# Kernel optimization log

Measured on AMD Instinct MI355X. Metric: run time of the kernel, lower is better.

## Reference

```python
import jax, jax.numpy as jnp
import numpy as np

# NTU RGB+D 25-joint skeleton edges (1-based)
NTU_EDGES = [(1,2),(2,21),(3,21),(4,3),(5,21),(6,5),(7,6),(8,7),(9,21),(10,9),
             (11,10),(12,11),(13,1),(14,13),(15,14),(16,15),(17,1),(18,17),
             (19,18),(20,19),(22,23),(23,8),(24,25),(25,12)]
NUM_SCALES = 13
NUM_POINT = 25


def build_A_powers(num_scales=NUM_SCALES, v=NUM_POINT):
    # MS-G3D disentangled multi-scale aggregation: exact-k-hop adjacencies, each
    # with self loops, symmetrically normalized, stacked along dim 0 -> (K*V, V).
    A = np.zeros((v, v))
    for i, j in NTU_EDGES:
        A[i - 1, j - 1] = 1.0
        A[j - 1, i - 1] = 1.0
    I = np.eye(v)
    mats = []
    for k in range(num_scales):
        if k == 0:
            Ak = I.copy()
        else:
            Ak = np.minimum(np.linalg.matrix_power(A + I, k), 1) \
               - np.minimum(np.linalg.matrix_power(A + I, k - 1), 1)
            Ak = Ak + I  # with_self=True
        d = Ak.sum(-1)
        dinv = np.where(d > 0, d ** -0.5, 0.0)
        mats.append((dinv[:, None] * Ak) * dinv[None, :])
    return np.concatenate(mats, 0).astype(np.float32)


def batchnorm(x, g, b, axes, ch_axis, eps=1e-5):
    # torch BatchNorm in training mode: biased batch stats + affine
    mean = jnp.mean(x, axes, keepdims=True)
    var = jnp.mean((x - mean) ** 2, axes, keepdims=True)
    shape = [1] * x.ndim
    shape[ch_axis] = -1
    return (x - mean) * jax.lax.rsqrt(var + eps) * g.reshape(shape) + b.reshape(shape)


def ms_gcn(x, A_powers, A_res, W, b, g, beta, num_scales):
    # x: (N, C, T, V); A: (K*V, V)
    A = A_powers + A_res
    support = jnp.einsum('vu,nctu->nctv', A, x)            # (N, C, T, K*V)
    N, C, T, KV = support.shape
    V = KV // num_scales
    support = support.reshape(N, C, T, num_scales, V).transpose(0, 3, 1, 2, 4)
    support = support.reshape(N, num_scales * C, T, V)     # (N, K*C, T, V)
    out = jnp.einsum('oc,nctv->notv', W, support) + b[None, :, None, None]  # 1x1 conv
    out = batchnorm(out, g, beta, (0, 2, 3), 1)
    return jax.nn.relu(out)


def lstm(x, Wih, Whh, bih, bhh):
    # single-layer batch_first LSTM, zero initial state; torch gate order i,f,g,o
    B = x.shape[0]
    H = Whh.shape[1]
    xp = jnp.einsum('bsd,hd->bsh', x, Wih) + bih + bhh     # precompute input proj

    def step(carry, xt):
        h, c = carry
        gates = xt + h @ Whh.T
        i, f, g, o = jnp.split(gates, 4, axis=-1)
        c = jax.nn.sigmoid(f) * c + jax.nn.sigmoid(i) * jnp.tanh(g)
        h = jax.nn.sigmoid(o) * jnp.tanh(c)
        return (h, c), h

    init = (jnp.zeros((B, H), x.dtype), jnp.zeros((B, H), x.dtype))
    _, ys = jax.lax.scan(step, init, jnp.swapaxes(xp, 0, 1))
    return jnp.swapaxes(ys, 0, 1)                          # (B, S, H)


def logsig_rnn(x, n_segments, Wih, Whh, bih, bhh):
    # x: (B, T, d). Depth-2 log-signature per time segment + segment start point,
    # concatenated and fed to an LSTM (Logsig-RNN layer).
    B, T, d = x.shape
    t_vec = np.array([int(round(float(v))) for v in np.linspace(1, T, n_segments + 1)])
    starts = t_vec[:-1] - 1
    ends = t_vec[1:] - 1
    L = int((ends - starts).max()) + 1
    # pad segments to fixed length by repeating the last point (zero increments)
    idx = np.minimum(starts[:, None] + np.arange(L)[None, :], ends[:, None])  # (S, L)
    pts = x[:, idx, :]                                     # (B, S, L, d)
    rel = pts - pts[:, :, :1, :]
    inc = rel[:, :, -1, :]                                 # level-1: total increment
    dx = pts[:, :, 1:, :] - pts[:, :, :-1, :]
    Mm = jnp.einsum('bsli,bslj->bsij', rel[:, :, :-1, :], dx)
    iu, ju = np.triu_indices(d, k=1)
    levy = 0.5 * (Mm[:, :, iu, ju] - Mm[:, :, ju, iu])     # level-2 (Lyndon basis)
    feats = jnp.concatenate([x[:, starts, :], inc, levy], axis=-1)
    return lstm(feats, Wih, Whh, bih, bhh)


def setup_inputs() -> dict:
    key = jax.random.key(0)
    ks = iter(jax.random.split(key, 16))
    N, C, T, V, M = 2, 3, 100, 25, 2
    c1, c2, num_class, K = 96, 192, 60, NUM_SCALES

    def randn(shape, scale):
        return jax.random.normal(next(ks), shape, jnp.float32) * scale

    ls1 = c1 + c1 * (c1 - 1) // 2     # 4656
    ls2 = c2 + c2 * (c2 - 1) // 2     # 18528
    in1 = c1 + ls1                    # 4752
    in2 = c2 + ls2                    # 18720
    Ap = jnp.asarray(build_A_powers())
    return {
        'x': jax.random.normal(next(ks), (N, C, T, V, M), jnp.float32),
        'length': jax.random.randint(next(ks), (N,), 0, T),
        'data_bn_g': jnp.ones((M * V * C,)), 'data_bn_b': jnp.zeros((M * V * C,)),
        'A_powers1': Ap,
        'A_res1': jax.random.uniform(next(ks), Ap.shape, jnp.float32, -1e-6, 1e-6),
        'W1': randn((c1, K * C), (K * C) ** -0.5), 'b1': jnp.zeros((c1,)),
        'bn1_g': jnp.ones((c1,)), 'bn1_b': jnp.zeros((c1,)),
        'Wih1': randn((4 * c1, in1), in1 ** -0.5), 'Whh1': randn((4 * c1, c1), c1 ** -0.5),
        'bih1': jnp.zeros((4 * c1,)), 'bhh1': jnp.zeros((4 * c1,)),
        'bnseg1_g': jnp.ones((50,)), 'bnseg1_b': jnp.zeros((50,)),
        'A_powers2': Ap,
        'A_res2': jax.random.uniform(next(ks), Ap.shape, jnp.float32, -1e-6, 1e-6),
        'W2': randn((c2, K * c1), (K * c1) ** -0.5), 'b2': jnp.zeros((c2,)),
        'bn2_g': jnp.ones((c2,)), 'bn2_b': jnp.zeros((c2,)),
        'Wih2': randn((4 * c2, in2), in2 ** -0.5), 'Whh2': randn((4 * c2, c2), c2 ** -0.5),
        'bih2': jnp.zeros((4 * c2,)), 'bhh2': jnp.zeros((4 * c2,)),
        'bnseg2_g': jnp.ones((30,)), 'bnseg2_b': jnp.zeros((30,)),
        'fcW': randn((num_class, c2), c2 ** -0.5), 'fcb': jnp.zeros((num_class,)),
    }


def reference(x, length, data_bn_g, data_bn_b, A_powers1, A_res1, W1, b1, bn1_g, bn1_b,
              Wih1, Whh1, bih1, bhh1, bnseg1_g, bnseg1_b, A_powers2, A_res2, W2, b2,
              bn2_g, bn2_b, Wih2, Whh2, bih2, bhh2, bnseg2_g, bnseg2_b, fcW, fcb):
    # `length` is accepted but unused, as in the original forward.
    N, C, T, V, M = x.shape
    K = A_powers1.shape[0] // V
    c1, c2 = W1.shape[0], W2.shape[0]
    S1, S2 = 50, 30

    h = x.transpose(0, 4, 3, 1, 2).reshape(N, M * V * C, T)
    h = batchnorm(h, data_bn_g, data_bn_b, (0, 2), 1)
    h = h.reshape(N * M, V, C, T).transpose(0, 2, 3, 1)            # (NM, C, T, V)

    h = jax.nn.relu(ms_gcn(h, A_powers1, A_res1, W1, b1, bn1_g, bn1_b, K))
    h = h.transpose(0, 3, 2, 1).reshape(N * M * V, T, c1)
    h = logsig_rnn(h, S1, Wih1, Whh1, bih1, bhh1)                  # (NMV, S1, c1)
    h = batchnorm(h, bnseg1_g, bnseg1_b, (0, 2), 1)
    h = h.reshape(N * M, V, S1, c1).transpose(0, 3, 2, 1)          # (NM, c1, S1, V)

    h = jax.nn.relu(ms_gcn(h, A_powers2, A_res2, W2, b2, bn2_g, bn2_b, K))
    h = h.transpose(0, 3, 2, 1).reshape(N * M * V, S1, c2)
    h = logsig_rnn(h, S2, Wih2, Whh2, bih2, bhh2)                  # (NMV, S2, c2)
    h = batchnorm(h, bnseg2_g, bnseg2_b, (0, 2), 1)
    h = h.reshape(N * M, V, S2, c2).transpose(0, 3, 2, 1)          # (NM, c2, S2, V)

    pooled = h.reshape(N, M, c2, -1).mean(axis=3).mean(axis=1)     # (N, c2)
    return pooled @ fcW.T + fcb
```

## Files before the change

### kernel.cpp

```cpp
#include <hip/hip_runtime.h>
#include <cmath>
#include <cstdint>
#include <cstddef>

typedef unsigned short bf16_t;
typedef __attribute__((ext_vector_type(8))) short short8;
typedef __attribute__((ext_vector_type(4))) float floatx4;
typedef __attribute__((ext_vector_type(2))) _Float16 half2_t;
typedef __attribute__((ext_vector_type(8))) _Float16 half8_t;

__device__ __forceinline__ float bf2f(bf16_t b){
  unsigned int u = ((unsigned int)b) << 16;
  return __uint_as_float(u);
}
__device__ __forceinline__ bf16_t f2bf(float f){
  unsigned int u = __float_as_uint(f);
  unsigned int r = (u + 0x7fffu + ((u >> 16) & 1u)) >> 16;
  return (bf16_t)r;
}
__device__ __forceinline__ unsigned int f2bf2(float a, float b){
  return (unsigned int)f2bf(a) | ((unsigned int)f2bf(b) << 16);
}
__device__ __forceinline__ float sigf(float x){ return 1.0f / (1.0f + expf(-x)); }

__device__ __forceinline__ float dot2(half2_t a, half2_t b, float c){
#if __has_builtin(__builtin_amdgcn_fdot2)
  return __builtin_amdgcn_fdot2(a, b, c, false);
#else
  return c + (float)a.x * (float)b.x + (float)a.y * (float)b.y;
#endif
}

__device__ __forceinline__ void gload_lds16(const bf16_t* g, bf16_t* lds){
  __builtin_amdgcn_global_load_lds(
      (const __attribute__((address_space(1))) unsigned int*)g,
      (__attribute__((address_space(3))) unsigned int*)lds, 16, 0, 0);
}

__device__ __forceinline__ void barrier_raw(){
  asm volatile("s_barrier" ::: "memory");
}

__device__ __forceinline__ int xcd_chunk_swizzle(int orig, int nwg){
  int q = nwg >> 3, r = nwg & 7;
  int xcd = orig & 7, idx = orig >> 3;
  return (xcd < r ? xcd * (q + 1) : r * (q + 1) + (xcd - r) * q) + idx;
}

__global__ void prep_misc(const float* __restrict__ a1, const float* __restrict__ r1, float* __restrict__ o1,
                          const float* __restrict__ a2, const float* __restrict__ r2, float* __restrict__ o2,
                          const float* __restrict__ bi1, const float* __restrict__ bh1, float* __restrict__ ob1,
                          const float* __restrict__ bi2, const float* __restrict__ bh2, float* __restrict__ ob2,
                          const float* __restrict__ Whh1, half2_t* __restrict__ Wp1,
                          const float* __restrict__ Whh2, half2_t* __restrict__ Wp2,
                          unsigned short* __restrict__ lut1, unsigned short* __restrict__ lut2,
                          float* __restrict__ stats, bf16_t* __restrict__ A2mat){
  int i = blockIdx.x * blockDim.x + threadIdx.x;
  if (i < 8125){ o1[i] = a1[i] + r1[i]; o2[i] = a2[i] + r2[i]; }
  if (i < 384) ob1[i] = bi1[i] + bh1[i];
  if (i < 768) ob2[i] = bi2[i] + bh2[i];
  if (i < 736) stats[i] = 0.f;
  if (i < 18432){
    int t = i % 384, j2 = i / 384;
    half2_t w; w.x = (_Float16)Whh1[(size_t)t * 96 + 2 * j2];
    w.y = (_Float16)Whh1[(size_t)t * 96 + 2 * j2 + 1];
    Wp1[i] = w;
  }
  if (i < 73728){
    int t = i % 768, j2 = i / 768;
    half2_t w; w.x = (_Float16)Whh2[(size_t)t * 192 + 2 * j2];
    w.y = (_Float16)Whh2[(size_t)t * 192 + 2 * j2 + 1];
    Wp2[i] = w;
  }
  if (i < 4560){
    int d = 96, p = i;
    int r = (int)(((2.0 * d - 1.0) - sqrt((2.0 * d - 1.0) * (2.0 * d - 1.0) - 8.0 * (double)p)) * 0.5);
    if (r < 0) r = 0;
    while (r + 1 <= d - 2 && (r + 1) * (d - 1) - ((r + 1) * r) / 2 <= p) ++r;
    while (r > 0 && r * (d - 1) - (r * (r - 1)) / 2 > p) --r;
    int jj = p - (r * (d - 1) - (r * (r - 1)) / 2);
    lut1[p] = (unsigned short)((r << 8) | (r + 1 + jj));
  }
  if (i < 18336){
    int d = 192, p = i;
    int r = (int)(((2.0 * d - 1.0) - sqrt((2.0 * d - 1.0) * (2.0 * d - 1.0) - 8.0 * (double)p)) * 0.5);
    if (r < 0) r = 0;
    while (r + 1 <= d - 2 && (r + 1) * (d - 1) - ((r + 1) * r) / 2 <= p) ++r;
    while (r > 0 && r * (d - 1) - (r * (r - 1)) / 2 > p) --r;
    int jj = p - (r * (d - 1) - (r * (r - 1)) / 2);
    lut2[p] = (unsigned short)((r << 8) | (r + 1 + jj));
  }
  if (i < 160000){
    int row = i >> 5, col = 1248 + (i & 31);
    A2mat[(size_t)row * 1280 + col] = 0;
  }
}

__device__ __forceinline__ void f2bf_seg(const float* in, bf16_t* out, int Kin, int Kout, int li){
  int ko8 = Kout >> 3;
  int r = li / ko8, k8 = (li % ko8) << 3;
  uint4 u;
  if (k8 + 8 <= Kin){
    const float4* p = reinterpret_cast<const float4*>(in + (size_t)r * Kin + k8);
    float4 x0 = p[0], x1 = p[1];
    u.x = f2bf2(x0.x, x0.y); u.y = f2bf2(x0.z, x0.w);
    u.z = f2bf2(x1.x, x1.y); u.w = f2bf2(x1.z, x1.w);
  } else {
    u.x = u.y = u.z = u.w = 0u;
  }
  *reinterpret_cast<uint4*>(out + (size_t)r * Kout + k8) = u;
}

__global__ void f2bf_pad8_3(const float* __restrict__ in1, bf16_t* __restrict__ out1, int Kin1, int Kout1, int c1,
                            const float* __restrict__ in2, bf16_t* __restrict__ out2, int Kin2, int Kout2, int c2,
                            const float* __restrict__ in3, bf16_t* __restrict__ out3, int Kin3, int Kout3, int c3){
  int idx = blockIdx.x * blockDim.x + threadIdx.x;
  if (idx < c1){ f2bf_seg(in1, out1, Kin1, Kout1, idx); return; }
  idx -= c1;
  if (idx < c2){ f2bf_seg(in2, out2, Kin2, Kout2, idx); return; }
  idx -= c2;
  if (idx < c3) f2bf_seg(in3, out3, Kin3, Kout3, idx);
}

__global__ void data_bn_kernel(const float* __restrict__ x, const float* __restrict__ g,
                               const float* __restrict__ bb, float* __restrict__ h1,
                               int N, int C, int T, int V, int M){
  int ch = blockIdx.x;
  int m = ch / (V * C);
  int v = (ch / C) % V;
  int c = ch % C;
  int tid = threadIdx.x;
  int cnt = N * T;
  float s = 0.f, s2 = 0.f;
  for (int i = tid; i < cnt; i += 64){
    int n = i / T, t = i % T;
    float val = x[(((size_t)(n * C + c) * T + t) * V + v) * M + m];
    s += val; s2 += val * val;
  }
  for (int off = 32; off; off >>= 1){ s += __shfl_down(s, off); s2 += __shfl_down(s2, off); }
  s = __shfl(s, 0); s2 = __shfl(s2, 0);
  float mean = s / cnt;
  float rstd = rsqrtf(s2 / cnt - mean * mean + 1e-5f);
  float gg = g[ch], bo = bb[ch];
  for (int i = tid; i < cnt; i += 64){
    int n = i / T, t = i % T;
    float val = x[(((size_t)(n * C + c) * T + t) * V + v) * M + m];
    float y = (val - mean) * rstd * gg + bo;
    h1[((size_t)((n * M + m) * C + c) * T + t) * V + v] = y;
  }
}

__global__ __launch_bounds__(256)
void gcn1_fused(const float* __restrict__ A, const float* __restrict__ h1,
                const float* __restrict__ W1, const float* __restrict__ b1,
                float* __restrict__ y1, float* __restrict__ ssum, float* __restrict__ ssq, int T){
  __shared__ float h[3][25];
  __shared__ float sup[3][325];
  __shared__ float lsum[96], lsq[96];
  int blk = blockIdx.x;
  int nm = blk / T, t = blk % T;
  int tid = threadIdx.x;
  if (tid < 75){
    int c = tid / 25, v = tid % 25;
    h[c][v] = h1[((size_t)(nm * 3 + c) * T + t) * 25 + v];
  }
  if (tid < 96){ lsum[tid] = 0.f; lsq[tid] = 0.f; }
  __syncthreads();
  for (int w = tid; w < 975; w += 256){
    int c = w / 325, ww = w % 325;
    const float* ar = A + ww * 25;
    float acc = 0.f;
    #pragma unroll
    for (int u = 0; u < 25; ++u) acc += ar[u] * h[c][u];
    sup[c][ww] = acc;
  }
  __syncthreads();
  for (int o2 = tid; o2 < 2400; o2 += 256){
    int v = o2 / 96, o = o2 % 96;
    float acc = b1[o];
    #pragma unroll
    for (int k = 0; k < 13; ++k)
      #pragma unroll
      for (int c = 0; c < 3; ++c)
        acc += W1[o * 39 + k * 3 + c] * sup[c][k * 25 + v];
    y1[((size_t)blk * 25 + v) * 96 + o] = acc;
    atomicAdd(&lsum[o], acc);
    atomicAdd(&lsq[o], acc * acc);
  }
  __syncthreads();
  if (tid < 96){ atomicAdd(&ssum[tid], lsum[tid]); atomicAdd(&ssq[tid], lsq[tid]); }
}

struct SegTable { int st[50]; int en[50]; };

__global__ void feats_bn_kernel(const float* __restrict__ ymat, const float* __restrict__ sum,
                                const float* __restrict__ sumsq, const float* __restrict__ g,
                                const float* __restrict__ bb, bf16_t* __restrict__ feats,
                                SegTable segs, const unsigned int* __restrict__ lut32,
                                int T, int d, int S, int L, int pairs, int rowlenP, int R){
  __shared__ float pts[4][192];
  int bs = blockIdx.x;
  int b = bs / S, s = bs % S;
  int nm = b / 25, v = b % 25;
  int st = segs.st[s], en = segs.en[s];
  int nt = blockDim.x, tid = threadIdx.x;
  for (int l = 0; l < L; ++l){
    int t = st + l; if (t > en) t = en;
    const float* yrow = ymat + ((size_t)(nm * T + t) * 25 + v) * d;
    for (int i = tid; i < d; i += nt){
      float mean = sum[i] / R;
      float rstd = rsqrtf(sumsq[i] / R - mean * mean + 1e-5f);
      pts[l][i] = fmaxf((yrow[i] - mean) * rstd * g[i] + bb[i], 0.f);
    }
  }
  __syncthreads();
  unsigned int* frow32 = reinterpret_cast<unsigned int*>(feats + (size_t)bs * rowlenP);
  int d2 = d >> 1;
  for (int i2 = tid; i2 < d2; i2 += nt){
    int i = 2 * i2;
    frow32[i2]      = f2bf2(pts[0][i], pts[0][i + 1]);
    frow32[d2 + i2] = f2bf2(pts[L - 1][i] - pts[0][i], pts[L - 1][i + 1] - pts[0][i + 1]);
  }
  int rowlen2 = (2 * d + pairs) >> 1, rowlenP2 = rowlenP >> 1;
  for (int i = tid + rowlen2; i < rowlenP2; i += nt) frow32[i] = 0;
  int Lm2 = L - 2;
  unsigned int* lrow32 = frow32 + d;
  int pairs2 = pairs >> 1;
  for (int p2 = tid; p2 < pairs2; p2 += nt){
    unsigned int ee = lut32[p2];
    int i0 = (ee >> 8) & 255, j0 = ee & 255;
    int i1 = ee >> 24, j1 = (ee >> 16) & 255;
    float acc0 = 0.f, acc1 = 0.f;
    for (int l = 1; l <= Lm2; ++l){
      float ri = pts[l][i0] - pts[0][i0], rj = pts[l][j0] - pts[0][j0];
      float di = pts[l + 1][i0] - pts[l][i0], dj = pts[l + 1][j0] - pts[l][j0];
      acc0 += ri * dj - rj * di;
      float ri1 = pts[l][i1] - pts[0][i1], rj1 = pts[l][j1] - pts[0][j1];
      float di1 = pts[l + 1][i1] - pts[l][i1], dj1 = pts[l + 1][j1] - pts[l][j1];
      acc1 += ri1 * dj1 - rj1 * di1;
    }
    lrow32[p2] = f2bf2(0.5f * acc0, 0.5f * acc1);
  }
}

__global__ __launch_bounds__(256)
void gemm_mfma_nt_split(const bf16_t* __restrict__ A, const bf16_t* __restrict__ B,
                        float* __restrict__ P, int M, int N, int K,
                        int GX, int GY, int GZ){
  __shared__ bf16_t As[128 * 64];
  __shared__ bf16_t Bs[128 * 64];
  const int nwg = GX * GY * GZ;
  const int wg = xcd_chunk_swizzle(blockIdx.x, nwg);
  const int bxi = wg % GX, byi = (wg / GX) % GY, bzi = wg / (GX * GY);
  const int tid = threadIdx.x;
  const int lane = tid & 63, wv = tid >> 6;
  const int bm = bxi * 128, bn = byi * 128;
  const int wr = (wv >> 1) * 64, wc = (wv & 1) * 64;
  const int m_l = lane & 15, q = lane >> 4;

  const int ksteps = K >> 6;
  const int Z = GZ, z = bzi;
  const int per = (ksteps + Z - 1) / Z;
  const int ks0 = z * per;
  const int ks1 = (ks0 + per < ksteps) ? ks0 + per : ksteps;

  const int rlane = lane >> 3;
  const int slane = lane & 7;
  const int colc = (slane ^ rlane) * 8;
  const bf16_t* gA[4]; const bf16_t* gB[4];
  bf16_t* lA[4]; bf16_t* lB[4];
  #pragma unroll
  for (int it = 0; it < 4; ++it){
    int c = it * 4 + wv;
    int rowA = bm + c * 8 + rlane; if (rowA > M - 1) rowA = M - 1;
    int rowB = bn + c * 8 + rlane; if (rowB > N - 1) rowB = N - 1;
    gA[it] = A + (size_t)rowA * K + colc;
    gB[it] = B + (size_t)rowB * K + colc;
    lA[it] = &As[c * 512];
    lB[it] = &Bs[c * 512];
  }
  const int sxor = m_l & 7;

  floatx4 acc[4][4] = {};
  for (int ks = ks0; ks < ks1; ++ks){
    int k0 = ks << 6;
    __syncthreads();
    #pragma unroll
    for (int it = 0; it < 4; ++it){
      gload_lds16(gA[it] + k0, lA[it]);
      gload_lds16(gB[it] + k0, lB[it]);
    }
    __syncthreads();
    #pragma unroll
    for (int half = 0; half < 2; ++half){
      const int scol = ((half * 4 + q) ^ sxor) * 8;
      short8 af[4], bfr[4];
      #pragma unroll
      for (int i = 0; i < 4; ++i){
        af[i]  = *reinterpret_cast<const short8*>(&As[(wr + i * 16 + m_l) * 64 + scol]);
        bfr[i] = *reinterpret_cast<const short8*>(&Bs[(wc + i * 16 + m_l) * 64 + scol]);
      }
      #pragma unroll
      for (int mi = 0; mi < 4; ++mi)
        #pragma unroll
        for (int ni = 0; ni < 4; ++ni)
          acc[mi][ni] = __builtin_amdgcn_mfma_f32_16x16x32_bf16(af[mi], bfr[ni], acc[mi][ni], 0, 0, 0);
    }
  }

  float* Pz = P + (size_t)z * M * N;
  #pragma unroll
  for (int mi = 0; mi < 4; ++mi){
    int row0 = bm + wr + mi * 16 + q * 4;
    #pragma unroll
    for (int r = 0; r < 4; ++r){
      int row = row0 + r;
      if (row < M){
        #pragma unroll
        for (int ni = 0; ni < 4; ++ni){
          int col = bn + wc + ni * 16 + m_l;
          if (col < N) Pz[(size_t)row * N + col] = acc[mi][ni][r];
        }
      }
    }
  }
}

#define VMC4 asm volatile("s_waitcnt vmcnt(4)" ::: "memory")
#define VMC0 asm volatile("s_waitcnt vmcnt(0)" ::: "memory")
#define STG4(NB, KH, OFF) { gload_lds16(pA0 + (OFF) + (KH) * 32, dA0 + (NB) * 16384 + (KH) * 8192); \
                            gload_lds16(pA1 + (OFF) + (KH) * 32, dA1 + (NB) * 16384 + (KH) * 8192); \
                            gload_lds16(pB0 + (OFF) + (KH) * 32, dB0 + (NB) * 16384 + (KH) * 8192); \
                            gload_lds16(pB1 + (OFF) + (KH) * 32, dB1 + (NB) * 16384 + (KH) * 8192); }
#define HP(BUF, KH, STAGE_BLOCK, WAIT_BLOCK) { \
    const bf16_t* ab_ = As + (BUF) * 16384 + (KH) * 8192 + sA; \
    _Pragma("unroll") \
    for (int i_ = 0; i_ < 8; ++i_) af[i_] = *reinterpret_cast<const short8*>(ab_ + i_ * 512); \
    const bf16_t* bb_ = Bs + (BUF) * 16384 + (KH) * 8192 + sB; \
    _Pragma("unroll") \
    for (int i_ = 0; i_ < 4; ++i_) bfr[i_] = *reinterpret_cast<const short8*>(bb_ + i_ * 512); \
    STAGE_BLOCK; \
    WAIT_BLOCK; \
    barrier_raw(); \
    __builtin_amdgcn_s_setprio(1); \
    _Pragma("unroll") \
    for (int mi_ = 0; mi_ < 8; ++mi_) \
      _Pragma("unroll") \
      for (int ni_ = 0; ni_ < 4; ++ni_) \
        acc[mi_][ni_] = __builtin_amdgcn_mfma_f32_16x16x32_bf16(af[mi_], bfr[ni_], acc[mi_][ni_], 0, 0, 0); \
    __builtin_amdgcn_s_setprio(0); \
  }

__global__ __launch_bounds__(512, 2)
void gemm_mfma_nt_8ph(const bf16_t* __restrict__ A, const bf16_t* __restrict__ B,
                      float* __restrict__ P, int M, int N, int K,
                      int GX, int GY, int GZ){
  __shared__ bf16_t As[32768];
  __shared__ bf16_t Bs[32768];
  const int nwg = GX * GY * GZ;
  const int wg = xcd_chunk_swizzle(blockIdx.x, nwg);
  const int bxi = wg % GX, byi = (wg / GX) % GY, bzi = wg / (GX * GY);
  const int tid = threadIdx.x;
  const int lane = tid & 63, wv = tid >> 6;
  const int wm = wv >> 2, wn = wv & 3;
  const int m_l = lane & 15, q = lane >> 4;
  const int bm = bxi * 256, bn = byi * 256;

  const int ksteps = K >> 6;
  const int z = bzi, Z = GZ;
  const int per = (ksteps + Z - 1) / Z;
  const int ks0 = z * per;
  int ks1 = ks0 + per; if (ks1 > ksteps) ks1 = ksteps;
  if (ks0 >= ks1) return;

  const int rlane = lane >> 2, slane = lane & 3;
  const int cg = slane ^ ((rlane >> 1) & 3);
  int rr0 = wv * 16 + rlane, rr1 = (8 + wv) * 16 + rlane;
  int ra0 = bm + rr0; if (ra0 > M - 1) ra0 = M - 1;
  int ra1 = bm + rr1; if (ra1 > M - 1) ra1 = M - 1;
  int rb0 = bn + rr0; if (rb0 > N - 1) rb0 = N - 1;
  int rb1 = bn + rr1; if (rb1 > N - 1) rb1 = N - 1;
  const bf16_t* pA0 = A + (size_t)ra0 * K + cg * 8 + ks0 * 64;
  const bf16_t* pA1 = A + (size_t)ra1 * K + cg * 8 + ks0 * 64;
  const bf16_t* pB0 = B + (size_t)rb0 * K + cg * 8 + ks0 * 64;
  const bf16_t* pB1 = B + (size_t)rb1 * K + cg * 8 + ks0 * 64;
  bf16_t* dA0 = As + wv * 512;
  bf16_t* dA1 = As + (8 + wv) * 512;
  bf16_t* dB0 = Bs + wv * 512;
  bf16_t* dB1 = Bs + (8 + wv) * 512;

  const int sA = (wm * 128 + m_l) * 32 + ((q ^ ((m_l >> 1) & 3)) * 8);
  const int sB = (wn * 64 + m_l) * 32 + ((q ^ ((m_l >> 1) & 3)) * 8);

  short8 af[8], bfr[4];
  floatx4 acc[8][4] = {};

  STG4(0, 0, 0); STG4(0, 1, 0);
  VMC4;
  barrier_raw();

  int buf = 0;
  for (int t = ks0; t < ks1 - 1; ++t){
    const int nb = buf ^ 1;
    HP(buf, 0, STG4(nb, 0, 64), VMC4);
    HP(buf, 1, STG4(nb, 1, 64), VMC4);
    pA0 += 64; pA1 += 64; pB0 += 64; pB1 += 64;
    buf = nb;
  }
  HP(buf, 0, ((void)0), VMC0);
  HP(buf, 1, ((void)0), ((void)0));

  float* Pz = P + (size_t)z * M * N;
  #pragma unroll
  for (int mi = 0; mi < 8; ++mi){
    int row0 = bm + wm * 128 + mi * 16 + q * 4;
    #pragma unroll
    for (int r = 0; r < 4; ++r){
      int row = row0 + r;
      if (row < M){
        #pragma unroll
        for (int ni = 0; ni < 4; ++ni){
          int col = bn + wn * 64 + ni * 16 + m_l;
          if (col < N) Pz[(size_t)row * N + col] = acc[mi][ni][r];
        }
      }
    }
  }
}

__global__ __launch_bounds__(256)
void reduce_split_bias_stats(const float* __restrict__ P, const float* __restrict__ bias,
                             float* __restrict__ out, float* __restrict__ ssum, float* __restrict__ ssq,
                             int MN, int N, int Z){
  __shared__ float lsum[192], lsq[192];
  int tid = threadIdx.x;
  if (tid < 192){ lsum[tid] = 0.f; lsq[tid] = 0.f; }
  __syncthreads();
  int i4 = (blockIdx.x * blockDim.x + tid) * 4;
  if (i4 < MN){
    const float4 bv = *reinterpret_cast<const float4*>(bias + (i4 % N));
    float4 s = bv;
    for (int z = 0; z < Z; ++z){
      const float4 p = *reinterpret_cast<const float4*>(P + (size_t)z * MN + i4);
      s.x += p.x; s.y += p.y; s.z += p.z; s.w += p.w;
    }
    *reinterpret_cast<float4*>(out + i4) = s;
    int c0 = i4 % N;
    atomicAdd(&lsum[c0],     s.x); atomicAdd(&lsq[c0],     s.x * s.x);
    atomicAdd(&lsum[c0 + 1], s.y); atomicAdd(&lsq[c0 + 1], s.y * s.y);
    atomicAdd(&lsum[c0 + 2], s.z); atomicAdd(&lsq[c0 + 2], s.z * s.z);
    atomicAdd(&lsum[c0 + 3], s.w); atomicAdd(&lsq[c0 + 3], s.w * s.w);
  }
  __syncthreads();
  if (tid < 192){ atomicAdd(&ssum[tid], lsum[tid]); atomicAdd(&ssq[tid], lsq[tid]); }
}

template <int H2C, int BLK, int Z>
__global__ __launch_bounds__(BLK, 1)
void lstm_kernel(const float* __restrict__ P, const float* __restrict__ bias,
                 const half2_t* __restrict__ Wp, float* __restrict__ out,
                 int S, int MN){
  constexpr int H = 2 * H2C;
  constexpr int H4 = 4 * H;
  __shared__ _Float16 __attribute__((aligned(16))) hsh[H];
  __shared__ float gv[H4];
  __shared__ float av[H4];
  const int b = blockIdx.x, t = threadIdx.x;
  half2_t w[H2C];
  const half2_t* wp = Wp + t;
  #pragma unroll
  for (int j2 = 0; j2 < H2C; ++j2) w[j2] = wp[(size_t)j2 * H4];
  float cc = 0.f;
  if (t < H) hsh[t] = (_Float16)0.f;
  const float bval = bias[t];
  const size_t base = (size_t)b * S * H4 + t;
  float pv0[Z], pv1[Z];
  #pragma unroll
  for (int z = 0; z < Z; ++z) pv0[z] = P[(size_t)z * MN + base];
  #pragma unroll
  for (int z = 0; z < Z; ++z) pv1[z] = P[(size_t)z * MN + base + H4];
  __syncthreads();
  const half8_t* hp8 = reinterpret_cast<const half8_t*>(hsh);
  for (int s = 0; s < S; ++s){
    float pvn[Z];
    if (s + 2 < S){
      size_t o2 = base + (size_t)(s + 2) * H4;
      #pragma unroll
      for (int z = 0; z < Z; ++z) pvn[z] = P[(size_t)z * MN + o2];
    }
    float a0 = bval, a1 = 0.f, a2 = 0.f, a3 = 0.f;
    float a4 = 0.f, a5 = 0.f, a6 = 0.f, a7 = 0.f;
    #pragma unroll
    for (int z = 0; z < Z; ++z) a0 += pv0[z];
    #pragma unroll
    for (int j8 = 0; j8 < H2C / 8; ++j8){
      half8_t hv0 = hp8[2 * j8];
      half8_t hv1 = hp8[2 * j8 + 1];
      half2_t h0, h1, h2, h3, h4, h5, h6, h7;
      h0.x = hv0[0]; h0.y = hv0[1];
      h1.x = hv0[2]; h1.y = hv0[3];
      h2.x = hv0[4]; h2.y = hv0[5];
      h3.x = hv0[6]; h3.y = hv0[7];
      h4.x = hv1[0]; h4.y = hv1[1];
      h5.x = hv1[2]; h5.y = hv1[3];
      h6.x = hv1[4]; h6.y = hv1[5];
      h7.x = hv1[6]; h7.y = hv1[7];
      const int jb = 8 * j8;
      a0 = dot2(w[jb],     h0, a0);
      a1 = dot2(w[jb + 1], h1, a1);
      a2 = dot2(w[jb + 2], h2, a2);
      a3 = dot2(w[jb + 3], h3, a3);
      a4 = dot2(w[jb + 4], h4, a4);
      a5 = dot2(w[jb + 5], h5, a5);
      a6 = dot2(w[jb + 6], h6, a6);
      a7 = dot2(w[jb + 7], h7, a7);
    }
    gv[t] = ((a0 + a1) + (a2 + a3)) + ((a4 + a5) + (a6 + a7));
    __syncthreads();
    {
      float x = gv[t];
      av[t] = (t >= 2 * H && t < 3 * H) ? tanhf(x) : sigf(x);
    }
    __syncthreads();
    if (t < H){
      float ig = av[t];
      float fg = av[H + t];
      float gg = av[2 * H + t];
      float og = av[3 * H + t];
      cc = fg * cc + ig * gg;
      float hh = og * tanhf(cc);
      hsh[t] = (_Float16)hh;
      out[((size_t)b * S + s) * H + t] = hh;
    }
    __syncthreads();
    #pragma unroll
    for (int z = 0; z < Z; ++z){ pv0[z] = pv1[z]; pv1[z] = pvn[z]; }
  }
}

__global__ __launch_bounds__(256)
void seg_stats_kernel(const float* __restrict__ lout, float* __restrict__ ssum,
                      float* __restrict__ ssq, int S, int H, int B){
  int s = blockIdx.x;
  int tid = threadIdx.x;
  int cnt = B * H;
  float a = 0.f, b2 = 0.f;
  for (int i = tid; i < cnt; i += 256){
    int b = i / H, o = i % H;
    float v = lout[((size_t)b * S + s) * H + o];
    a += v; b2 += v * v;
  }
  for (int off = 32; off; off >>= 1){ a += __shfl_down(a, off); b2 += __shfl_down(b2, off); }
  __shared__ float sa[4], sb[4];
  int wid = tid >> 6, lane = tid & 63;
  if (lane == 0){ sa[wid] = a; sb[wid] = b2; }
  __syncthreads();
  if (tid == 0){
    ssum[s] = (sa[0] + sa[1]) + (sa[2] + sa[3]);
    ssq[s]  = (sb[0] + sb[1]) + (sb[2] + sb[3]);
  }
}

__global__ void support2_bn(const float* __restrict__ A, const float* __restrict__ lout,
                            const float* __restrict__ ssum, const float* __restrict__ ssq,
                            const float* __restrict__ g, const float* __restrict__ bb,
                            bf16_t* __restrict__ A2mat, int S, int cnt){
  int idx = blockIdx.x * blockDim.x + threadIdx.x;
  int total = 4 * S * 25 * 13 * 96;
  if (idx >= total) return;
  int c = idx % 96;
  int k = (idx / 96) % 13;
  int v = (idx / (96 * 13)) % 25;
  int rs = idx / (96 * 13 * 25);
  int s = rs % S, nm = rs / S;
  float mean = ssum[s] / cnt;
  float rstd = rsqrtf(ssq[s] / cnt - mean * mean + 1e-5f);
  float scale = rstd * g[s];
  float shift = bb[s] - mean * scale;
  const float* ar = A + (k * 25 + v) * 25;
  float acc = 0.f;
  #pragma unroll
  for (int u = 0; u < 25; ++u){
    float raw = lout[((size_t)(nm * 25 + u) * S + s) * 96 + c];
    acc += ar[u] * (raw * scale + shift);
  }
  A2mat[((size_t)rs * 25 + v) * 1280 + k * 96 + c] = f2bf(acc);
}

__global__ void pool_kernel(const float* __restrict__ lout2, const float* __restrict__ sum,
                            const float* __restrict__ sumsq, const float* __restrict__ g,
                            const float* __restrict__ bb, float* __restrict__ pooled,
                            int S, int H, int scnt){
  int n = blockIdx.x / H;
  int o = blockIdx.x % H;
  float acc = 0.f;
  int cnt = 2 * 25 * S;
  for (int i = threadIdx.x; i < cnt; i += 64){
    int m = i / (25 * S);
    int r = i % (25 * S);
    int v = r / S;
    int s = r % S;
    int b = (n * 2 + m) * 25 + v;
    float val = lout2[((size_t)b * S + s) * H + o];
    float mean = sum[s] / scnt;
    float rstd = rsqrtf(sumsq[s] / scnt - mean * mean + 1e-5f);
    val = (val - mean) * rstd * g[s] + bb[s];
    acc += val;
  }
  for (int off = 32; off; off >>= 1) acc += __shfl_down(acc, off);
  if (threadIdx.x == 0) pooled[n * H + o] = acc / cnt;
}

__global__ void fc_kernel(const float* __restrict__ pooled, const float* __restrict__ fcW,
                          const float* __restrict__ fcb, float* __restrict__ outp){
  int idx = blockIdx.x * blockDim.x + threadIdx.x;
  if (idx >= 120) return;
  int n = idx / 60, cls = idx % 60;
  float acc = fcb[cls];
  for (int o = 0; o < 192; ++o) acc += pooled[n * 192 + o] * fcW[cls * 192 + o];
  outp[idx] = acc;
}

static void make_segs(int T, int S, SegTable& tab, int& L){
  double step = (double)(T - 1) / (double)S;
  long long tv[51];
  for (int i = 0; i <= S; ++i){
    double v = 1.0 + step * (double)i;
    tv[i] = llrint(v);
  }
  L = 0;
  for (int s = 0; s < S; ++s){
    tab.st[s] = (int)tv[s] - 1;
    tab.en[s] = (int)tv[s + 1] - 1;
    int len = tab.en[s] - tab.st[s] + 1;
    if (len > L) L = len;
  }
  for (int s = S; s < 50; ++s){ tab.st[s] = 0; tab.en[s] = 0; }
  if (L > 4) L = 4;
}

extern "C" void kernel_launch(void* const* d_in, const int* in_sizes, int n_in,
                              void* d_out, int out_size, void* d_ws, size_t ws_size,
                              hipStream_t stream){
  const float* x         = (const float*)d_in[0];
  const float* data_bn_g = (const float*)d_in[2];
  const float* data_bn_b = (const float*)d_in[3];
  const float* A_powers1 = (const float*)d_in[4];
  const float* A_res1    = (const float*)d_in[5];
  const float* W1        = (const float*)d_in[6];
  const float* b1        = (const float*)d_in[7];
  const float* bn1_g     = (const float*)d_in[8];
  const float* bn1_b     = (const float*)d_in[9];
  const float* Wih1      = (const float*)d_in[10];
  const float* Whh1      = (const float*)d_in[11];
  const float* bih1      = (const float*)d_in[12];
  const float* bhh1      = (const float*)d_in[13];
  const float* bnseg1_g  = (const float*)d_in[14];
  const float* bnseg1_b  = (const float*)d_in[15];
  const float* A_powers2 = (const float*)d_in[16];
  const float* A_res2    = (const float*)d_in[17];
  const float* W2        = (const float*)d_in[18];
  const float* b2        = (const float*)d_in[19];
  const float* bn2_g     = (const float*)d_in[20];
  const float* bn2_b     = (const float*)d_in[21];
  const float* Wih2      = (const float*)d_in[22];
  const float* Whh2      = (const float*)d_in[23];
  const float* bih2      = (const float*)d_in[24];
  const float* bhh2      = (const float*)d_in[25];
  const float* bnseg2_g  = (const float*)d_in[26];
  const float* bnseg2_b  = (const float*)d_in[27];
  const float* fcW       = (const float*)d_in[28];
  const float* fcb       = (const float*)d_in[29];
  float* out = (float*)d_out;

  const int N = 2, C = 3, T = 100, V = 25, M = 2, NM = 4;
  const int C1 = 96, C2 = 192;
  const int S1 = 50, S2 = 30;
  const int B = 100;
  const int IN1 = 4752, IN2 = 18720;
  const int IN1P = 4800, IN2P = 18752;
  const int P1 = 4560, P2 = 18336;
  const int KG2 = 1248, KG2P = 1280;
  const int Z1 = 6, Z2 = 7, ZG = 4;

  size_t off = 0;
  char* base = (char*)d_ws;
  auto alloc = [&](size_t nbytes) -> void* {
    off = (off + 255) & ~(size_t)255;
    void* p = base + off;
    off += nbytes;
    return p;
  };
  float* A1full = (float*)alloc(325 * 25 * 4);
  float* A2full = (float*)alloc(325 * 25 * 4);
  float* h1     = (float*)alloc((size_t)NM * C * T * V * 4);
  float* y1mat  = (float*)alloc((size_t)NM * T * V * C1 * 4);
  float* stats  = (float*)alloc(736 * 4);
  float* st1a = stats, *st1b = stats + 96;
  float* sg1a = stats + 192, *sg1b = stats + 242;
  float* st2a = stats + 292, *st2b = stats + 484;
  float* sg2a = stats + 676, *sg2b = stats + 706;
  float* l1out  = (float*)alloc((size_t)B * S1 * C1 * 4);
  bf16_t* A2mat = (bf16_t*)alloc((size_t)NM * S1 * V * KG2P * 2);
  float* y2mat  = (float*)alloc((size_t)NM * S1 * V * C2 * 4);
  float* l2out  = (float*)alloc((size_t)B * S2 * C2 * 4);
  float* pooled = (float*)alloc(2 * C2 * 4);
  float* bias1  = (float*)alloc(4 * C1 * 4);
  float* bias2  = (float*)alloc(4 * C2 * 4);
  half2_t* Wp1  = (half2_t*)alloc((size_t)(C1 / 2) * 4 * C1 * 4);
  half2_t* Wp2  = (half2_t*)alloc((size_t)(C2 / 2) * 4 * C2 * 4);
  bf16_t* Wih1b = (bf16_t*)alloc((size_t)4 * C1 * IN1P * 2);
  bf16_t* Wih2b = (bf16_t*)alloc((size_t)4 * C2 * IN2P * 2);
  bf16_t* W2b   = (bf16_t*)alloc((size_t)C2 * KG2P * 2);
  unsigned short* lut1 = (unsigned short*)alloc((size_t)P1 * 2);
  unsigned short* lut2 = (unsigned short*)alloc((size_t)P2 * 2);
  size_t pmax = (size_t)Z2 * 3000 * 768;
  {
    size_t p1s = (size_t)Z1 * 5000 * 384; if (p1s > pmax) pmax = p1s;
    size_t pgs = (size_t)ZG * 5000 * 192; if (pgs > pmax) pmax = pgs;
  }
  float* Pbuf = (float*)alloc(pmax * 4);
  bf16_t* feats = (bf16_t*)alloc((size_t)B * S2 * IN2P * 2);
  (void)ws_size; (void)in_sizes; (void)n_in; (void)out_size;

  prep_misc<<<625, 256, 0, stream>>>(A_powers1, A_res1, A1full, A_powers2, A_res2, A2full,
                                     bih1, bhh1, bias1, bih2, bhh2, bias2,
                                     Whh1, Wp1, Whh2, Wp2, lut1, lut2, stats, A2mat);
  {
    int c1 = 4 * C1 * (IN1P / 8);
    int c2 = 4 * C2 * (IN2P / 8);
    int c3 = C2 * (KG2P / 8);
    int tot = c1 + c2 + c3;
    f2bf_pad8_3<<<(tot + 255) / 256, 256, 0, stream>>>(Wih1, Wih1b, IN1, IN1P, c1,
                                                       Wih2, Wih2b, IN2, IN2P, c2,
                                                       W2, W2b, KG2, KG2P, c3);
  }

  data_bn_kernel<<<M * V * C, 64, 0, stream>>>(x, data_bn_g, data_bn_b, h1, N, C, T, V, M);

  gcn1_fused<<<NM * T, 256, 0, stream>>>(A1full, h1, W1, b1, y1mat, st1a, st1b, T);

  SegTable seg1, seg2; int L1, L2;
  make_segs(T, S1, seg1, L1);
  make_segs(S1, S2, seg2, L2);

  feats_bn_kernel<<<B * S1, 256, 0, stream>>>(y1mat, st1a, st1b, bn1_g, bn1_b, feats, seg1,
                                              (const unsigned int*)lut1, T, C1, S1, L1, P1, IN1P,
                                              NM * T * 25);
  {
    int Mm = B * S1, Nn = 4 * C1;
    int GX = (Mm + 255) / 256, GY = (Nn + 255) / 256;
    gemm_mfma_nt_8ph<<<GX * GY * Z1, 512, 0, stream>>>(feats, Wih1b, Pbuf, Mm, Nn, IN1P,
                                                       GX, GY, Z1);
    lstm_kernel<48, 384, Z1><<<B, 384, 0, stream>>>(Pbuf, bias1, Wp1, l1out, S1, Mm * Nn);
    seg_stats_kernel<<<S1, 256, 0, stream>>>(l1out, sg1a, sg1b, S1, C1, B);
  }

  {
    int tot = NM * S1 * 25 * 13 * 96;
    support2_bn<<<(tot + 255) / 256, 256, 0, stream>>>(A2full, l1out, sg1a, sg1b, bnseg1_g,
                                                       bnseg1_b, A2mat, S1, B * C1);
  }
  {
    int Mm = NM * S1 * 25, Nn = C2;
    int GX = (Mm + 127) / 128, GY = (Nn + 127) / 128;
    gemm_mfma_nt_split<<<GX * GY * ZG, 256, 0, stream>>>(A2mat, W2b, Pbuf, Mm, Nn, KG2P,
                                                         GX, GY, ZG);
    int MN = Mm * Nn;
    reduce_split_bias_stats<<<(MN / 4 + 255) / 256, 256, 0, stream>>>(Pbuf, b2, y2mat, st2a, st2b,
                                                                      MN, Nn, ZG);
  }

  feats_bn_kernel<<<B * S2, 256, 0, stream>>>(y2mat, st2a, st2b, bn2_g, bn2_b, feats, seg2,
                                              (const unsigned int*)lut2, S1, C2, S2, L2, P2, IN2P,
                                              NM * S1 * 25);
  {
    int Mm = B * S2, Nn = 4 * C2;
    int GX = (Mm + 255) / 256, GY = (Nn + 255) / 256;
    gemm_mfma_nt_8ph<<<GX * GY * Z2, 512, 0, stream>>>(feats, Wih2b, Pbuf, Mm, Nn, IN2P,
                                                       GX, GY, Z2);
    lstm_kernel<96, 768, Z2><<<B, 768, 0, stream>>>(Pbuf, bias2, Wp2, l2out, S2, Mm * Nn);
    seg_stats_kernel<<<S2, 256, 0, stream>>>(l2out, sg2a, sg2b, S2, C2, B);
  }

  pool_kernel<<<2 * C2, 64, 0, stream>>>(l2out, sg2a, sg2b, bnseg2_g, bnseg2_b, pooled, S2, C2, B * C2);
  fc_kernel<<<1, 128, 0, stream>>>(pooled, fcW, fcb, out);
}
```

Measured before the change: 643.7 us.

## Restructure 256x256 GEMM tile to 4 waves with 128x128 per-wave subtiles

The LSTM input-projection GEMM now uses 256 threads (4 waves, 2x2) instead of 512 (8 waves, 2x4), and each wave computes a 128x128 subtile with 8x8 MFMA accumulators. Staging loads are reorganized so each thread issues eight 16-byte global-to-LDS loads per half-step, and the wait count is raised to match. The aim is more MFMA work per LDS fragment read and fewer waves contending for barriers. In exchange, register pressure rises sharply (256 accumulator floats per lane) and occupancy drops to one block of 4 waves, which leaves less latency hiding.

```diff
diff --git a/kernel.cpp b/kernel.cpp
--- a/kernel.cpp
+++ b/kernel.cpp
@@ -326,19 +326,22 @@
   }
 }
 
-#define VMC4 asm volatile("s_waitcnt vmcnt(4)" ::: "memory")
+#define VMC8 asm volatile("s_waitcnt vmcnt(8)" ::: "memory")
 #define VMC0 asm volatile("s_waitcnt vmcnt(0)" ::: "memory")
-#define STG4(NB, KH, OFF) { gload_lds16(pA0 + (OFF) + (KH) * 32, dA0 + (NB) * 16384 + (KH) * 8192); \
-                            gload_lds16(pA1 + (OFF) + (KH) * 32, dA1 + (NB) * 16384 + (KH) * 8192); \
-                            gload_lds16(pB0 + (OFF) + (KH) * 32, dB0 + (NB) * 16384 + (KH) * 8192); \
-                            gload_lds16(pB1 + (OFF) + (KH) * 32, dB1 + (NB) * 16384 + (KH) * 8192); }
-#define HP(BUF, KH, STAGE_BLOCK, WAIT_BLOCK) { \
+#define STG8(NB, KH, OFF) { \
+    _Pragma("unroll") \
+    for (int j_ = 0; j_ < 4; ++j_) \
+      gload_lds16(pA[j_] + (OFF) + (KH) * 32, dA + (NB) * 16384 + (KH) * 8192 + j_ * 2048); \
+    _Pragma("unroll") \
+    for (int j_ = 0; j_ < 4; ++j_) \
+      gload_lds16(pB[j_] + (OFF) + (KH) * 32, dB + (NB) * 16384 + (KH) * 8192 + j_ * 2048); }
+#define HP8(BUF, KH, STAGE_BLOCK, WAIT_BLOCK) { \
     const bf16_t* ab_ = As + (BUF) * 16384 + (KH) * 8192 + sA; \
     _Pragma("unroll") \
     for (int i_ = 0; i_ < 8; ++i_) af[i_] = *reinterpret_cast<const short8*>(ab_ + i_ * 512); \
     const bf16_t* bb_ = Bs + (BUF) * 16384 + (KH) * 8192 + sB; \
     _Pragma("unroll") \
-    for (int i_ = 0; i_ < 4; ++i_) bfr[i_] = *reinterpret_cast<const short8*>(bb_ + i_ * 512); \
+    for (int i_ = 0; i_ < 8; ++i_) bfr[i_] = *reinterpret_cast<const short8*>(bb_ + i_ * 512); \
     STAGE_BLOCK; \
     WAIT_BLOCK; \
     barrier_raw(); \
@@ -346,12 +349,12 @@
     _Pragma("unroll") \
     for (int mi_ = 0; mi_ < 8; ++mi_) \
       _Pragma("unroll") \
-      for (int ni_ = 0; ni_ < 4; ++ni_) \
+      for (int ni_ = 0; ni_ < 8; ++ni_) \
         acc[mi_][ni_] = __builtin_amdgcn_mfma_f32_16x16x32_bf16(af[mi_], bfr[ni_], acc[mi_][ni_], 0, 0, 0); \
     __builtin_amdgcn_s_setprio(0); \
   }
 
-__global__ __launch_bounds__(512, 2)
+__global__ __launch_bounds__(256, 1)
 void gemm_mfma_nt_8ph(const bf16_t* __restrict__ A, const bf16_t* __restrict__ B,
                       float* __restrict__ P, int M, int N, int K,
                       int GX, int GY, int GZ){
@@ -362,7 +365,7 @@
   const int bxi = wg % GX, byi = (wg / GX) % GY, bzi = wg / (GX * GY);
   const int tid = threadIdx.x;
   const int lane = tid & 63, wv = tid >> 6;
-  const int wm = wv >> 2, wn = wv & 3;
+  const int wm = wv >> 1, wn = wv & 1;
   const int m_l = lane & 15, q = lane >> 4;
   const int bm = bxi * 256, bn = byi * 256;
 
@@ -373,42 +376,40 @@
   int ks1 = ks0 + per; if (ks1 > ksteps) ks1 = ksteps;
   if (ks0 >= ks1) return;
 
-  const int rlane = lane >> 2, slane = lane & 3;
-  const int cg = slane ^ ((rlane >> 1) & 3);
-  int rr0 = wv * 16 + rlane, rr1 = (8 + wv) * 16 + rlane;
-  int ra0 = bm + rr0; if (ra0 > M - 1) ra0 = M - 1;
-  int ra1 = bm + rr1; if (ra1 > M - 1) ra1 = M - 1;
-  int rb0 = bn + rr0; if (rb0 > N - 1) rb0 = N - 1;
-  int rb1 = bn + rr1; if (rb1 > N - 1) rb1 = N - 1;
-  const bf16_t* pA0 = A + (size_t)ra0 * K + cg * 8 + ks0 * 64;
-  const bf16_t* pA1 = A + (size_t)ra1 * K + cg * 8 + ks0 * 64;
-  const bf16_t* pB0 = B + (size_t)rb0 * K + cg * 8 + ks0 * 64;
-  const bf16_t* pB1 = B + (size_t)rb1 * K + cg * 8 + ks0 * 64;
-  bf16_t* dA0 = As + wv * 512;
-  bf16_t* dA1 = As + (8 + wv) * 512;
-  bf16_t* dB0 = Bs + wv * 512;
-  bf16_t* dB1 = Bs + (8 + wv) * 512;
+  const int t4 = tid >> 2, qt = tid & 3;
+  const int cg = qt ^ ((t4 >> 1) & 3);
+  const bf16_t* pA[4]; const bf16_t* pB[4];
+  #pragma unroll
+  for (int j = 0; j < 4; ++j){
+    int ra = bm + j * 64 + t4; if (ra > M - 1) ra = M - 1;
+    int rb = bn + j * 64 + t4; if (rb > N - 1) rb = N - 1;
+    pA[j] = A + (size_t)ra * K + cg * 8 + ks0 * 64;
+    pB[j] = B + (size_t)rb * K + cg * 8 + ks0 * 64;
+  }
+  bf16_t* dA = As + wv * 512;
+  bf16_t* dB = Bs + wv * 512;
 
   const int sA = (wm * 128 + m_l) * 32 + ((q ^ ((m_l >> 1) & 3)) * 8);
-  const int sB = (wn * 64 + m_l) * 32 + ((q ^ ((m_l >> 1) & 3)) * 8);
-
-  short8 af[8], bfr[4];
-  floatx4 acc[8][4] = {};
-
-  STG4(0, 0, 0); STG4(0, 1, 0);
-  VMC4;
+  const int sB = (wn * 128 + m_l) * 32 + ((q ^ ((m_l >> 1) & 3)) * 8);
+
+  short8 af[8], bfr[8];
+  floatx4 acc[8][8] = {};
+
+  STG8(0, 0, 0); STG8(0, 1, 0);
+  VMC8;
   barrier_raw();
 
   int buf = 0;
   for (int t = ks0; t < ks1 - 1; ++t){
     const int nb = buf ^ 1;
-    HP(buf, 0, STG4(nb, 0, 64), VMC4);
-    HP(buf, 1, STG4(nb, 1, 64), VMC4);
-    pA0 += 64; pA1 += 64; pB0 += 64; pB1 += 64;
+    HP8(buf, 0, STG8(nb, 0, 64), VMC8);
+    HP8(buf, 1, STG8(nb, 1, 64), VMC8);
+    #pragma unroll
+    for (int j = 0; j < 4; ++j){ pA[j] += 64; pB[j] += 64; }
     buf = nb;
   }
-  HP(buf, 0, ((void)0), VMC0);
-  HP(buf, 1, ((void)0), ((void)0));
+  HP8(buf, 0, ((void)0), VMC0);
+  HP8(buf, 1, ((void)0), ((void)0));
 
   float* Pz = P + (size_t)z * M * N;
   #pragma unroll
@@ -419,8 +420,8 @@
       int row = row0 + r;
       if (row < M){
         #pragma unroll
-        for (int ni = 0; ni < 4; ++ni){
-          int col = bn + wn * 64 + ni * 16 + m_l;
+        for (int ni = 0; ni < 8; ++ni){
+          int col = bn + wn * 128 + ni * 16 + m_l;
           if (col < N) Pz[(size_t)row * N + col] = acc[mi][ni][r];
         }
       }
@@ -750,7 +751,7 @@
   {
     int Mm = B * S1, Nn = 4 * C1;
     int GX = (Mm + 255) / 256, GY = (Nn + 255) / 256;
-    gemm_mfma_nt_8ph<<<GX * GY * Z1, 512, 0, stream>>>(feats, Wih1b, Pbuf, Mm, Nn, IN1P,
+    gemm_mfma_nt_8ph<<<GX * GY * Z1, 256, 0, stream>>>(feats, Wih1b, Pbuf, Mm, Nn, IN1P,
                                                        GX, GY, Z1);
     lstm_kernel<48, 384, Z1><<<B, 384, 0, stream>>>(Pbuf, bias1, Wp1, l1out, S1, Mm * Nn);
     seg_stats_kernel<<<S1, 256, 0, stream>>>(l1out, sg1a, sg1b, S1, C1, B);
@@ -777,7 +778,7 @@
   {
     int Mm = B * S2, Nn = 4 * C2;
     int GX = (Mm + 255) / 256, GY = (Nn + 255) / 256;
-    gemm_mfma_nt_8ph<<<GX * GY * Z2, 512, 0, stream>>>(feats, Wih2b, Pbuf, Mm, Nn, IN2P,
+    gemm_mfma_nt_8ph<<<GX * GY * Z2, 256, 0, stream>>>(feats, Wih2b, Pbuf, Mm, Nn, IN2P,
                                                        GX, GY, Z2);
     lstm_kernel<96, 768, Z2><<<B, 768, 0, stream>>>(Pbuf, bias2, Wp2, l2out, S2, Mm * Nn);
     seg_stats_kernel<<<S2, 256, 0, stream>>>(l2out, sg2a, sg2b, S2, C2, B);
```

After: 651.5 us. No clear change (+1.2%).
